# Kernel tuning notes

Hardware: AMD Instinct MI355X
Metric: run time of the kernel (lower is better)

Reference implementation:

```python
import jax, jax.numpy as jnp
import numpy as np

N = 500_000
N_GROUPS = 50_000
D_IN = 64
D_OUT = 64
IN_MLP = D_IN * 3  # x, x - min, x - max (use_num=False)
NEG_SLOPE = 0.2


def setup_inputs() -> dict:
    key = jax.random.key(0)
    k_x, k_c, k_w1, k_w2 = jax.random.split(key, 4)
    x = jax.random.normal(k_x, (N, D_IN), dtype=jnp.float32)
    # CSR pointer: 0 = p0 <= p1 <= ... <= p_{n_groups} = N
    inner = jnp.sort(jax.random.randint(k_c, (N_GROUPS - 1,), 0, N))
    csr_idx = jnp.concatenate([jnp.zeros((1,), jnp.int64 if jax.config.jax_enable_x64 else jnp.int32),
                               inner.astype(jnp.int32),
                               jnp.full((1,), N, jnp.int32)]).astype(jnp.int32)
    # MLP([in_mlp, d_out, d_out], bias=False): two bias-free Linear layers,
    # each followed by LeakyReLU(0.2) (BatchNorm omitted / identity).
    w1 = jax.random.normal(k_w1, (IN_MLP, D_OUT), dtype=jnp.float32) / np.sqrt(IN_MLP)
    w2 = jax.random.normal(k_w2, (D_OUT, D_OUT), dtype=jnp.float32) / np.sqrt(D_OUT)
    return {"x": x, "csr_idx": csr_idx, "w1": w1, "w2": w2}


def _forward(x, csr_idx, w1, w2):
    n = x.shape[0]
    # element -> segment id (jit-safe equivalent of repeat_interleave on lengths)
    seg = jnp.searchsorted(csr_idx, jnp.arange(n, dtype=csr_idx.dtype), side='right') - 1  # [N]
    # segment min/max + gather-back
    seg_min = jax.ops.segment_min(x, seg, num_segments=N_GROUPS)  # [G, D]
    seg_max = jax.ops.segment_max(x, seg, num_segments=N_GROUPS)  # [G, D]
    x_map_min = x - seg_min[seg]
    x_map_max = x - seg_max[seg]
    h = jnp.concatenate([x, x_map_min, x_map_max], axis=1)  # [N, 3*D_IN]
    h = jax.nn.leaky_relu(h @ w1, NEG_SLOPE)
    h = jax.nn.leaky_relu(h @ w2, NEG_SLOPE)
    return h


def reference(x, csr_idx, w1, w2):
    return _forward(x, csr_idx, w1, w2)
```

## Files before the change

### kernel.cpp

```cpp
#include <hip/hip_runtime.h>
#include <math.h>

#define NROWS 500000
#define NGRP  50000
#define NEG   0.2f
#define GPB   16

typedef __attribute__((ext_vector_type(8))) short bf16x8;
typedef __attribute__((ext_vector_type(4))) float f32x4;
typedef unsigned int uint32;

__device__ __forceinline__ float leaky(float h) { return fmaxf(h, NEG * h); }
__device__ __forceinline__ unsigned short f2bf(float v) {
    uint32 u = __float_as_uint(v);
    u += 0x7FFFu + ((u >> 16) & 1u);
    return (unsigned short)(u >> 16);
}
__device__ __forceinline__ float bf2f(unsigned short h) {
    return __uint_as_float((uint32)h << 16);
}
__device__ __forceinline__ uint32 pkbf(float a, float b) {
    uint32 r;
    asm("v_cvt_pk_bf16_f32 %0, %1, %2" : "=v"(r) : "v"(a), "v"(b));
    return r;
}

__global__ void k0_frag(const float* __restrict__ w1, const float* __restrict__ w2,
                        unsigned short* __restrict__ wsf, unsigned short* __restrict__ w2f,
                        unsigned short* __restrict__ wbh, unsigned short* __restrict__ wbl) {
    int r = blockIdx.x * 256 + threadIdx.x;
    if (r >= 8192) return;
    int j = r & 7, q = (r >> 3) & 3, n = (r >> 5) & 63;
    int k = (r >> 11) * 32 + q * 8 + j;
    if (r < 4096) {
        float ws = w1[k * 64 + n] + w1[4096 + k * 64 + n] + w1[8192 + k * 64 + n];
        wsf[r] = f2bf(ws);
        w2f[r] = f2bf(w2[k * 64 + n]);
    }
    float v = w1[(64 + k) * 64 + n];
    unsigned short h = f2bf(v);
    wbh[r] = h;
    wbl[r] = f2bf(v - bf2f(h));
}

__global__ __launch_bounds__(256, 6)
void grpstat(const float* __restrict__ x, const int* __restrict__ csr,
             const unsigned short* __restrict__ wbh,
             const unsigned short* __restrict__ wbl,
             float* __restrict__ biasG, int* __restrict__ seg) {
    __shared__ float mnF[GPB * 132];
    __shared__ int csrl[GPB + 1];

    const int tid = threadIdx.x, w = tid >> 6, lane = tid & 63;
    const int q = lane >> 4, nl = lane & 15;
    const int n = w * 16 + nl;

    const int g0 = blockIdx.x * GPB;
    if (tid <= GPB) csrl[tid] = csr[g0 + tid];
    __syncthreads();
    const int p0 = csrl[0], p1 = csrl[GPB];

    for (int r = p0 + tid; r < p1; r += 256) {
        int lo = 0, hi = GPB;
#pragma unroll
        for (int it = 0; it < 5; ++it) {
            int mid = (lo + hi) >> 1;
            bool cb = csrl[mid] <= r;
            lo = cb ? mid : lo;
            hi = cb ? hi : mid;
        }
        seg[r] = g0 + lo;
    }

    {
        const int sub = q;
        const float4* xr = (const float4*)x;

        auto redgrp = [&](int gl, int q0, int cnt,
                          float4 r0, float4 r1, float4 r2, float4 r3) {
            if (cnt <= 0) return;
            float4 mn, mx;
            mn.x = fminf(fminf(r0.x, r1.x), fminf(r2.x, r3.x));
            mn.y = fminf(fminf(r0.y, r1.y), fminf(r2.y, r3.y));
            mn.z = fminf(fminf(r0.z, r1.z), fminf(r2.z, r3.z));
            mn.w = fminf(fminf(r0.w, r1.w), fminf(r2.w, r3.w));
            mx.x = fmaxf(fmaxf(r0.x, r1.x), fmaxf(r2.x, r3.x));
            mx.y = fmaxf(fmaxf(r0.y, r1.y), fmaxf(r2.y, r3.y));
            mx.z = fmaxf(fmaxf(r0.z, r1.z), fmaxf(r2.z, r3.z));
            mx.w = fmaxf(fmaxf(r0.w, r1.w), fmaxf(r2.w, r3.w));
            for (int i = 16; i < cnt; i += 16) {
                int ra = q0 + min(i + sub,      cnt - 1);
                int rb = q0 + min(i + sub + 4,  cnt - 1);
                int rc = q0 + min(i + sub + 8,  cnt - 1);
                int rd = q0 + min(i + sub + 12, cnt - 1);
                float4 a = xr[ra * 16 + nl], b = xr[rb * 16 + nl];
                float4 c = xr[rc * 16 + nl], d = xr[rd * 16 + nl];
                mn.x = fminf(mn.x, fminf(fminf(a.x, b.x), fminf(c.x, d.x)));
                mn.y = fminf(mn.y, fminf(fminf(a.y, b.y), fminf(c.y, d.y)));
                mn.z = fminf(mn.z, fminf(fminf(a.z, b.z), fminf(c.z, d.z)));
                mn.w = fminf(mn.w, fminf(fminf(a.w, b.w), fminf(c.w, d.w)));
                mx.x = fmaxf(mx.x, fmaxf(fmaxf(a.x, b.x), fmaxf(c.x, d.x)));
                mx.y = fmaxf(mx.y, fmaxf(fmaxf(a.y, b.y), fmaxf(c.y, d.y)));
                mx.z = fmaxf(mx.z, fmaxf(fmaxf(a.z, b.z), fmaxf(c.z, d.z)));
                mx.w = fmaxf(mx.w, fmaxf(fmaxf(a.w, b.w), fmaxf(c.w, d.w)));
            }
#pragma unroll
            for (int mk = 16; mk <= 32; mk <<= 1) {
                mn.x = fminf(mn.x, __shfl_xor(mn.x, mk));
                mn.y = fminf(mn.y, __shfl_xor(mn.y, mk));
                mn.z = fminf(mn.z, __shfl_xor(mn.z, mk));
                mn.w = fminf(mn.w, __shfl_xor(mn.w, mk));
                mx.x = fmaxf(mx.x, __shfl_xor(mx.x, mk));
                mx.y = fmaxf(mx.y, __shfl_xor(mx.y, mk));
                mx.z = fmaxf(mx.z, __shfl_xor(mx.z, mk));
                mx.w = fmaxf(mx.w, __shfl_xor(mx.w, mk));
            }
            if (sub == 0) {
                *(float4*)&mnF[gl * 132 + nl * 4]      = mn;
                *(float4*)&mnF[gl * 132 + 64 + nl * 4] = mx;
            }
        };

#pragma unroll
        for (int pr = 0; pr < 2; ++pr) {
            const int gA = w + pr * 8, gB = gA + 4;
            int qA = csrl[gA], cA = csrl[gA + 1] - qA;
            int qB = csrl[gB], cB = csrl[gB + 1] - qB;
            const int bA = (cA > 0) ? qA : 0, iA = max(cA - 1, 0);
            const int bB = (cB > 0) ? qB : 0, iB = max(cB - 1, 0);
            float4 a0 = xr[(bA + min(sub,      iA)) * 16 + nl];
            float4 a1 = xr[(bA + min(sub + 4,  iA)) * 16 + nl];
            float4 a2 = xr[(bA + min(sub + 8,  iA)) * 16 + nl];
            float4 a3 = xr[(bA + min(sub + 12, iA)) * 16 + nl];
            float4 b0 = xr[(bB + min(sub,      iB)) * 16 + nl];
            float4 b1 = xr[(bB + min(sub + 4,  iB)) * 16 + nl];
            float4 b2 = xr[(bB + min(sub + 8,  iB)) * 16 + nl];
            float4 b3 = xr[(bB + min(sub + 12, iB)) * 16 + nl];
            redgrp(gA, qA, cA, a0, a1, a2, a3);
            redgrp(gB, qB, cB, b0, b1, b2, b3);
        }
    }
    __syncthreads();

    {
        const bf16x8* bhv = (const bf16x8*)wbh;
        const bf16x8* blv = (const bf16x8*)wbl;
        f32x4 acc = { 0.f, 0.f, 0.f, 0.f };
#pragma unroll
        for (int ks = 0; ks < 4; ++ks) {
            bf16x8 Bh = bhv[(ks * 64 + n) * 4 + q];
            bf16x8 Bl = blv[(ks * 64 + n) * 4 + q];
            const float* ap = &mnF[nl * 132 + ks * 32 + q * 8];
            f32x4 v0 = *(const f32x4*)ap;
            f32x4 v1 = *(const f32x4*)(ap + 4);
            union U { bf16x8 v; uint32 u[4]; } ah, al;
            ah.u[0] = pkbf(v0[0], v0[1]);
            ah.u[1] = pkbf(v0[2], v0[3]);
            ah.u[2] = pkbf(v1[0], v1[1]);
            ah.u[3] = pkbf(v1[2], v1[3]);
            float r0 = v0[0] - __uint_as_float(ah.u[0] << 16);
            float r1 = v0[1] - __uint_as_float(ah.u[0] & 0xffff0000u);
            float r2 = v0[2] - __uint_as_float(ah.u[1] << 16);
            float r3 = v0[3] - __uint_as_float(ah.u[1] & 0xffff0000u);
            float r4 = v1[0] - __uint_as_float(ah.u[2] << 16);
            float r5 = v1[1] - __uint_as_float(ah.u[2] & 0xffff0000u);
            float r6 = v1[2] - __uint_as_float(ah.u[3] << 16);
            float r7 = v1[3] - __uint_as_float(ah.u[3] & 0xffff0000u);
            al.u[0] = pkbf(r0, r1);
            al.u[1] = pkbf(r2, r3);
            al.u[2] = pkbf(r4, r5);
            al.u[3] = pkbf(r6, r7);
            acc = __builtin_amdgcn_mfma_f32_16x16x32_bf16(ah.v, Bh, acc, 0, 0, 0);
            acc = __builtin_amdgcn_mfma_f32_16x16x32_bf16(al.v, Bh, acc, 0, 0, 0);
            acc = __builtin_amdgcn_mfma_f32_16x16x32_bf16(ah.v, Bl, acc, 0, 0, 0);
        }
#pragma unroll
        for (int r = 0; r < 4; ++r)
            biasG[(size_t)(g0 + q * 4 + r) * 64 + n] = -acc[r];
    }
}

__global__ __launch_bounds__(256, 6)
void mlp(const float* __restrict__ x, const int* __restrict__ seg,
         const float* __restrict__ biasG,
         const unsigned short* __restrict__ wsf,
         const unsigned short* __restrict__ w2f,
         float* __restrict__ out) {
    __shared__ __align__(16) short xb[64 * 72];
    __shared__ __align__(16) short y1s[64 * 72];
    __shared__ __align__(16) int rowgrpL[64];

    const int tid = threadIdx.x, w = tid >> 6, lane = tid & 63;
    const int q = lane >> 4, nl = lane & 15;
    const int n = w * 16 + nl;

    const int r0 = blockIdx.x * 64;
    const int rows = min(64, NROWS - r0);
    const int availf = rows * 64;

    const float4* x4 = (const float4*)(x + (size_t)r0 * 64);
#pragma unroll
    for (int i = 0; i < 4; ++i) {
        int f = (i * 256 + tid) * 4;
        if (f < availf) {
            float4 v = x4[f >> 2];
            int r = f >> 6, c = f & 63;
            uint2 p;
            p.x = pkbf(v.x, v.y);
            p.y = pkbf(v.z, v.w);
            *(uint2*)(&xb[r * 72 + c]) = p;
        }
    }
    if (tid < 64) rowgrpL[tid] = seg[min(r0 + tid, NROWS - 1)];

    const bf16x8* wsv = (const bf16x8*)wsf;
    const bf16x8* w2v = (const bf16x8*)w2f;
    bf16x8 B0 = wsv[n * 4 + q];
    bf16x8 B1 = wsv[(64 + n) * 4 + q];
    bf16x8 C0 = w2v[n * 4 + q];
    bf16x8 C1 = w2v[(64 + n) * 4 + q];
    __syncthreads();

    f32x4 h[4];
#pragma unroll
    for (int mt = 0; mt < 4; ++mt) {
        int rbase = mt * 16 + q * 4;
        int4 grp = *(const int4*)(&rowgrpL[rbase]);
        f32x4 acc;
        acc.x = biasG[(size_t)grp.x * 64 + n];
        acc.y = biasG[(size_t)grp.y * 64 + n];
        acc.z = biasG[(size_t)grp.z * 64 + n];
        acc.w = biasG[(size_t)grp.w * 64 + n];
        bf16x8 a0 = *(const bf16x8*)(&xb[(mt * 16 + nl) * 72 + q * 8]);
        bf16x8 a1 = *(const bf16x8*)(&xb[(mt * 16 + nl) * 72 + 32 + q * 8]);
        acc = __builtin_amdgcn_mfma_f32_16x16x32_bf16(a0, B0, acc, 0, 0, 0);
        acc = __builtin_amdgcn_mfma_f32_16x16x32_bf16(a1, B1, acc, 0, 0, 0);
        h[mt] = acc;
    }
#pragma unroll
    for (int mt = 0; mt < 4; ++mt) {
        int rbase = mt * 16 + q * 4;
        uint32 p01 = pkbf(leaky(h[mt][0]), leaky(h[mt][1]));
        uint32 p23 = pkbf(leaky(h[mt][2]), leaky(h[mt][3]));
        y1s[(rbase + 0) * 72 + n] = (short)(p01 & 0xffffu);
        y1s[(rbase + 1) * 72 + n] = (short)(p01 >> 16);
        y1s[(rbase + 2) * 72 + n] = (short)(p23 & 0xffffu);
        y1s[(rbase + 3) * 72 + n] = (short)(p23 >> 16);
    }
    __syncthreads();

#pragma unroll
    for (int mt = 0; mt < 4; ++mt) {
        f32x4 acc = {0.f, 0.f, 0.f, 0.f};
        bf16x8 a0 = *(const bf16x8*)(&y1s[(mt * 16 + nl) * 72 + q * 8]);
        bf16x8 a1 = *(const bf16x8*)(&y1s[(mt * 16 + nl) * 72 + 32 + q * 8]);
        acc = __builtin_amdgcn_mfma_f32_16x16x32_bf16(a0, C0, acc, 0, 0, 0);
        acc = __builtin_amdgcn_mfma_f32_16x16x32_bf16(a1, C1, acc, 0, 0, 0);
        int rbase = mt * 16 + q * 4;
#pragma unroll
        for (int r = 0; r < 4; ++r) {
            int rl = rbase + r;
            if (rl < rows)
                out[(size_t)(r0 + rl) * 64 + n] = leaky(acc[r]);
        }
    }
}

extern "C" void kernel_launch(void* const* d_in, const int* in_sizes, int n_in,
                              void* d_out, int out_size, void* d_ws, size_t ws_size,
                              hipStream_t stream) {
    const float* x   = (const float*)d_in[0];
    const int*   csr = (const int*)d_in[1];
    const float* w1  = (const float*)d_in[2];
    const float* w2  = (const float*)d_in[3];
    float* out = (float*)d_out;

    unsigned short* wsf = (unsigned short*)d_ws;
    unsigned short* w2f = wsf + 4096;
    unsigned short* wbh = wsf + 8192;
    unsigned short* wbl = wsf + 16384;
    float* biasG = (float*)((char*)d_ws + 49152);
    int*   seg   = (int*)((char*)d_ws + 49152 + 12800000);

    k0_frag<<<32, 256, 0, stream>>>(w1, w2, wsf, w2f, wbh, wbl);
    grpstat<<<NGRP / GPB, 256, 0, stream>>>(x, csr, wbh, wbl, biasG, seg);
    mlp<<<(NROWS + 63) / 64, 256, 0, stream>>>(x, seg, biasG, wsf, w2f, out);
}
```

Baseline: 260.3 us.

## Fuse group-stat and MLP into one persistent cooperative kernel with prefetch

```diff
diff --git a/kernel.cpp b/kernel.cpp
--- a/kernel.cpp
+++ b/kernel.cpp
@@ -1,10 +1,13 @@
 #include <hip/hip_runtime.h>
+#include <hip/hip_cooperative_groups.h>
 #include <math.h>
 
 #define NROWS 500000
 #define NGRP  50000
 #define NEG   0.2f
 #define GPB   16
+#define NCHG  3125
+#define NCHR  7813
 
 typedef __attribute__((ext_vector_type(8))) short bf16x8;
 typedef __attribute__((ext_vector_type(4))) float f32x4;
@@ -43,22 +46,19 @@
     wbl[r] = f2bf(v - bf2f(h));
 }
 
-__global__ __launch_bounds__(256, 6)
-void grpstat(const float* __restrict__ x, const int* __restrict__ csr,
-             const unsigned short* __restrict__ wbh,
-             const unsigned short* __restrict__ wbl,
-             float* __restrict__ biasG, int* __restrict__ seg) {
-    __shared__ float mnF[GPB * 132];
-    __shared__ int csrl[GPB + 1];
-
-    const int tid = threadIdx.x, w = tid >> 6, lane = tid & 63;
-    const int q = lane >> 4, nl = lane & 15;
-    const int n = w * 16 + nl;
-
-    const int g0 = blockIdx.x * GPB;
+
+__device__ __forceinline__ void phase1_chunk(
+        int gc, const float* __restrict__ x, const int* __restrict__ csr,
+        const unsigned short* __restrict__ wbh,
+        const unsigned short* __restrict__ wbl,
+        float* __restrict__ biasG, int* __restrict__ seg,
+        float* mnF, int* csrl,
+        int tid, int w, int q, int nl, int n) {
+    const int g0 = gc * GPB;
     if (tid <= GPB) csrl[tid] = csr[g0 + tid];
     __syncthreads();
     const int p0 = csrl[0], p1 = csrl[GPB];
+    const float4* xr = (const float4*)x;
 
     for (int r = p0 + tid; r < p1; r += 256) {
         int lo = 0, hi = GPB;
@@ -74,8 +74,6 @@
 
     {
         const int sub = q;
-        const float4* xr = (const float4*)x;
-
         auto redgrp = [&](int gl, int q0, int cnt,
                           float4 r0, float4 r1, float4 r2, float4 r3) {
             if (cnt <= 0) return;
@@ -120,7 +118,6 @@
                 *(float4*)&mnF[gl * 132 + 64 + nl * 4] = mx;
             }
         };
-
 #pragma unroll
         for (int pr = 0; pr < 2; ++pr) {
             const int gA = w + pr * 8, gB = gA + 4;
@@ -180,30 +177,21 @@
     }
 }
 
-__global__ __launch_bounds__(256, 6)
-void mlp(const float* __restrict__ x, const int* __restrict__ seg,
-         const float* __restrict__ biasG,
-         const unsigned short* __restrict__ wsf,
-         const unsigned short* __restrict__ w2f,
-         float* __restrict__ out) {
-    __shared__ __align__(16) short xb[64 * 72];
-    __shared__ __align__(16) short y1s[64 * 72];
-    __shared__ __align__(16) int rowgrpL[64];
-
-    const int tid = threadIdx.x, w = tid >> 6, lane = tid & 63;
-    const int q = lane >> 4, nl = lane & 15;
-    const int n = w * 16 + nl;
-
-    const int r0 = blockIdx.x * 64;
+__device__ __forceinline__ void phase2_chunk(
+        int rc, int rn, float4 stg[4], const float* __restrict__ x,
+        const int* __restrict__ seg, const float* __restrict__ biasG,
+        bf16x8 B0, bf16x8 B1, bf16x8 C0, bf16x8 C1,
+        float* __restrict__ out, short* xb, short* y1s, int* rowgrpL,
+        int tid, int q, int nl, int n) {
+    const int r0 = rc * 64;
     const int rows = min(64, NROWS - r0);
     const int availf = rows * 64;
 
-    const float4* x4 = (const float4*)(x + (size_t)r0 * 64);
 #pragma unroll
     for (int i = 0; i < 4; ++i) {
         int f = (i * 256 + tid) * 4;
         if (f < availf) {
-            float4 v = x4[f >> 2];
+            float4 v = stg[i];
             int r = f >> 6, c = f & 63;
             uint2 p;
             p.x = pkbf(v.x, v.y);
@@ -212,16 +200,18 @@
         }
     }
     if (tid < 64) rowgrpL[tid] = seg[min(r0 + tid, NROWS - 1)];
-
-    const bf16x8* wsv = (const bf16x8*)wsf;
-    const bf16x8* w2v = (const bf16x8*)w2f;
-    bf16x8 B0 = wsv[n * 4 + q];
-    bf16x8 B1 = wsv[(64 + n) * 4 + q];
-    bf16x8 C0 = w2v[n * 4 + q];
-    bf16x8 C1 = w2v[(64 + n) * 4 + q];
     __syncthreads();
 
-    f32x4 h[4];
+    if (rn >= 0) {
+        const int availn = min(64, NROWS - rn * 64) * 64;
+        const float4* x4 = (const float4*)(x + (size_t)rn * 64 * 64);
+#pragma unroll
+        for (int i = 0; i < 4; ++i) {
+            int f = (i * 256 + tid) * 4;
+            if (f < availn) stg[i] = x4[f >> 2];
+        }
+    }
+
 #pragma unroll
     for (int mt = 0; mt < 4; ++mt) {
         int rbase = mt * 16 + q * 4;
@@ -235,13 +225,8 @@
         bf16x8 a1 = *(const bf16x8*)(&xb[(mt * 16 + nl) * 72 + 32 + q * 8]);
         acc = __builtin_amdgcn_mfma_f32_16x16x32_bf16(a0, B0, acc, 0, 0, 0);
         acc = __builtin_amdgcn_mfma_f32_16x16x32_bf16(a1, B1, acc, 0, 0, 0);
-        h[mt] = acc;
-    }
-#pragma unroll
-    for (int mt = 0; mt < 4; ++mt) {
-        int rbase = mt * 16 + q * 4;
-        uint32 p01 = pkbf(leaky(h[mt][0]), leaky(h[mt][1]));
-        uint32 p23 = pkbf(leaky(h[mt][2]), leaky(h[mt][3]));
+        uint32 p01 = pkbf(leaky(acc[0]), leaky(acc[1]));
+        uint32 p23 = pkbf(leaky(acc[2]), leaky(acc[3]));
         y1s[(rbase + 0) * 72 + n] = (short)(p01 & 0xffffu);
         y1s[(rbase + 1) * 72 + n] = (short)(p01 >> 16);
         y1s[(rbase + 2) * 72 + n] = (short)(p23 & 0xffffu);
@@ -264,6 +249,110 @@
                 out[(size_t)(r0 + rl) * 64 + n] = leaky(acc[r]);
         }
     }
+}
+
+__global__ __launch_bounds__(256, 6)
+void both(const float* __restrict__ x, const int* __restrict__ csr,
+          const unsigned short* __restrict__ wbh,
+          const unsigned short* __restrict__ wbl,
+          const unsigned short* __restrict__ wsf,
+          const unsigned short* __restrict__ w2f,
+          float* __restrict__ biasG, int* __restrict__ seg,
+          float* __restrict__ out) {
+    __shared__ __align__(16) char smem[18944];
+    float* mnF  = (float*)smem;
+    int*   csrl = (int*)(smem + 8448);
+    short* xb   = (short*)smem;
+    short* y1s  = (short*)(smem + 9216);
+    int*   rowgrpL = (int*)(smem + 18432);
+
+    const int tid = threadIdx.x, w = tid >> 6, lane = tid & 63;
+    const int q = lane >> 4, nl = lane & 15;
+    const int n = w * 16 + nl;
+    const int bid = blockIdx.x, gsz = gridDim.x;
+
+    for (int gc = bid; gc < NCHG; gc += gsz) {
+        phase1_chunk(gc, x, csr, wbh, wbl, biasG, seg, mnF, csrl,
+                     tid, w, q, nl, n);
+        __syncthreads();
+    }
+
+    int rc = bid;
+    float4 stg[4];
+    if (rc < NCHR) {
+        const int availf = min(64, NROWS - rc * 64) * 64;
+        const float4* x4 = (const float4*)(x + (size_t)rc * 64 * 64);
+#pragma unroll
+        for (int i = 0; i < 4; ++i) {
+            int f = (i * 256 + tid) * 4;
+            if (f < availf) stg[i] = x4[f >> 2];
+        }
+    }
+
+    __threadfence();
+    cooperative_groups::this_grid().sync();
+
+    const bf16x8* wsv = (const bf16x8*)wsf;
+    const bf16x8* w2v = (const bf16x8*)w2f;
+    bf16x8 B0 = wsv[n * 4 + q];
+    bf16x8 B1 = wsv[(64 + n) * 4 + q];
+    bf16x8 C0 = w2v[n * 4 + q];
+    bf16x8 C1 = w2v[(64 + n) * 4 + q];
+
+    while (rc < NCHR) {
+        int rn = rc + gsz;
+        phase2_chunk(rc, rn < NCHR ? rn : -1, stg, x, seg, biasG,
+                     B0, B1, C0, C1, out, xb, y1s, rowgrpL, tid, q, nl, n);
+        rc = rn;
+    }
+}
+
+__global__ __launch_bounds__(256, 6)
+void grpstat(const float* __restrict__ x, const int* __restrict__ csr,
+             const unsigned short* __restrict__ wbh,
+             const unsigned short* __restrict__ wbl,
+             float* __restrict__ biasG, int* __restrict__ seg) {
+    __shared__ __align__(16) float mnF[GPB * 132];
+    __shared__ int csrl[GPB + 1];
+    const int tid = threadIdx.x, w = tid >> 6, lane = tid & 63;
+    const int q = lane >> 4, nl = lane & 15;
+    const int n = w * 16 + nl;
+    phase1_chunk(blockIdx.x, x, csr, wbh, wbl, biasG, seg, mnF, csrl,
+                 tid, w, q, nl, n);
+}
+
+__global__ __launch_bounds__(256, 6)
+void mlp(const float* __restrict__ x, const int* __restrict__ seg,
+         const float* __restrict__ biasG,
+         const unsigned short* __restrict__ wsf,
+         const unsigned short* __restrict__ w2f,
+         float* __restrict__ out) {
+    __shared__ __align__(16) short xb[64 * 72];
+    __shared__ __align__(16) short y1s[64 * 72];
+    __shared__ __align__(16) int rowgrpL[64];
+    const int tid = threadIdx.x, w = tid >> 6, lane = tid & 63;
+    const int q = lane >> 4, nl = lane & 15;
+    const int n = w * 16 + nl;
+    const int rc = blockIdx.x;
+
+    float4 stg[4];
+    {
+        const int availf = min(64, NROWS - rc * 64) * 64;
+        const float4* x4 = (const float4*)(x + (size_t)rc * 64 * 64);
+#pragma unroll
+        for (int i = 0; i < 4; ++i) {
+            int f = (i * 256 + tid) * 4;
+            if (f < availf) stg[i] = x4[f >> 2];
+        }
+    }
+    const bf16x8* wsv = (const bf16x8*)wsf;
+    const bf16x8* w2v = (const bf16x8*)w2f;
+    bf16x8 B0 = wsv[n * 4 + q];
+    bf16x8 B1 = wsv[(64 + n) * 4 + q];
+    bf16x8 C0 = w2v[n * 4 + q];
+    bf16x8 C1 = w2v[(64 + n) * 4 + q];
+    phase2_chunk(rc, -1, stg, x, seg, biasG, B0, B1, C0, C1, out,
+                 xb, y1s, rowgrpL, tid, q, nl, n);
 }
 
 extern "C" void kernel_launch(void* const* d_in, const int* in_sizes, int n_in,
@@ -283,6 +372,35 @@
     int*   seg   = (int*)((char*)d_ws + 49152 + 12800000);
 
     k0_frag<<<32, 256, 0, stream>>>(w1, w2, wsf, w2f, wbh, wbl);
-    grpstat<<<NGRP / GPB, 256, 0, stream>>>(x, csr, wbh, wbl, biasG, seg);
-    mlp<<<(NROWS + 63) / 64, 256, 0, stream>>>(x, seg, biasG, wsf, w2f, out);
-}
+
+    static int coopGrid = -2;
+    if (coopGrid == -2) {
+        int nb = 0, ncu = 0, dev = 0;
+        if (hipGetDevice(&dev) == hipSuccess &&
+            hipDeviceGetAttribute(&ncu, hipDeviceAttributeMultiprocessorCount,
+                                  dev) == hipSuccess &&
+            hipOccupancyMaxActiveBlocksPerMultiprocessor(
+                &nb, (const void*)both, 256, 0) == hipSuccess &&
+            nb > 0 && ncu > 0) {
+            long g = (long)nb * ncu;
+            coopGrid = (int)(g < 1536 ? g : 1536);
+        } else {
+            coopGrid = -1;
+        }
+    }
+
+    bool launched = false;
+    if (coopGrid > 0) {
+        void* args[] = { (void*)&x, (void*)&csr, (void*)&wbh, (void*)&wbl,
+                         (void*)&wsf, (void*)&w2f, (void*)&biasG, (void*)&seg,
+                         (void*)&out };
+        launched = hipLaunchCooperativeKernel((const void*)both, dim3(coopGrid),
+                                              dim3(256), args, 0, stream)
+                   == hipSuccess;
+        if (!launched) coopGrid = -1;
+    }
+    if (!launched) {
+        grpstat<<<NCHG, 256, 0, stream>>>(x, csr, wbh, wbl, biasG, seg);
+        mlp<<<NCHR, 256, 0, stream>>>(x, seg, biasG, wsf, w2f, out);
+    }
+}
```

Result: slower. 450.0 us (+72.9%).

## Make MLP kernel persistent with register prefetch of next x tile

Applied to the files above, without the earlier changes.

```diff
diff --git a/kernel.cpp b/kernel.cpp
--- a/kernel.cpp
+++ b/kernel.cpp
@@ -5,6 +5,9 @@
 #define NGRP  50000
 #define NEG   0.2f
 #define GPB   16
+#define NCHG  3125
+#define NCHR  7813
+#define GRID2 1954
 
 typedef __attribute__((ext_vector_type(8))) short bf16x8;
 typedef __attribute__((ext_vector_type(4))) float f32x4;
@@ -43,22 +46,18 @@
     wbl[r] = f2bf(v - bf2f(h));
 }
 
-__global__ __launch_bounds__(256, 6)
-void grpstat(const float* __restrict__ x, const int* __restrict__ csr,
-             const unsigned short* __restrict__ wbh,
-             const unsigned short* __restrict__ wbl,
-             float* __restrict__ biasG, int* __restrict__ seg) {
-    __shared__ float mnF[GPB * 132];
-    __shared__ int csrl[GPB + 1];
-
-    const int tid = threadIdx.x, w = tid >> 6, lane = tid & 63;
-    const int q = lane >> 4, nl = lane & 15;
-    const int n = w * 16 + nl;
-
-    const int g0 = blockIdx.x * GPB;
+__device__ __forceinline__ void phase1_chunk(
+        int gc, const float* __restrict__ x, const int* __restrict__ csr,
+        const unsigned short* __restrict__ wbh,
+        const unsigned short* __restrict__ wbl,
+        float* __restrict__ biasG, int* __restrict__ seg,
+        float* mnF, int* csrl,
+        int tid, int w, int q, int nl, int n) {
+    const int g0 = gc * GPB;
     if (tid <= GPB) csrl[tid] = csr[g0 + tid];
     __syncthreads();
     const int p0 = csrl[0], p1 = csrl[GPB];
+    const float4* xr = (const float4*)x;
 
     for (int r = p0 + tid; r < p1; r += 256) {
         int lo = 0, hi = GPB;
@@ -74,8 +73,6 @@
 
     {
         const int sub = q;
-        const float4* xr = (const float4*)x;
-
         auto redgrp = [&](int gl, int q0, int cnt,
                           float4 r0, float4 r1, float4 r2, float4 r3) {
             if (cnt <= 0) return;
@@ -120,7 +117,6 @@
                 *(float4*)&mnF[gl * 132 + 64 + nl * 4] = mx;
             }
         };
-
 #pragma unroll
         for (int pr = 0; pr < 2; ++pr) {
             const int gA = w + pr * 8, gB = gA + 4;
@@ -181,6 +177,20 @@
 }
 
 __global__ __launch_bounds__(256, 6)
+void grpstat(const float* __restrict__ x, const int* __restrict__ csr,
+             const unsigned short* __restrict__ wbh,
+             const unsigned short* __restrict__ wbl,
+             float* __restrict__ biasG, int* __restrict__ seg) {
+    __shared__ __align__(16) float mnF[GPB * 132];
+    __shared__ int csrl[GPB + 1];
+    const int tid = threadIdx.x, w = tid >> 6, lane = tid & 63;
+    const int q = lane >> 4, nl = lane & 15;
+    const int n = w * 16 + nl;
+    phase1_chunk(blockIdx.x, x, csr, wbh, wbl, biasG, seg, mnF, csrl,
+                 tid, w, q, nl, n);
+}
+
+__global__ __launch_bounds__(256, 4)
 void mlp(const float* __restrict__ x, const int* __restrict__ seg,
          const float* __restrict__ biasG,
          const unsigned short* __restrict__ wsf,
@@ -188,30 +198,11 @@
          float* __restrict__ out) {
     __shared__ __align__(16) short xb[64 * 72];
     __shared__ __align__(16) short y1s[64 * 72];
-    __shared__ __align__(16) int rowgrpL[64];
 
     const int tid = threadIdx.x, w = tid >> 6, lane = tid & 63;
     const int q = lane >> 4, nl = lane & 15;
     const int n = w * 16 + nl;
-
-    const int r0 = blockIdx.x * 64;
-    const int rows = min(64, NROWS - r0);
-    const int availf = rows * 64;
-
-    const float4* x4 = (const float4*)(x + (size_t)r0 * 64);
-#pragma unroll
-    for (int i = 0; i < 4; ++i) {
-        int f = (i * 256 + tid) * 4;
-        if (f < availf) {
-            float4 v = x4[f >> 2];
-            int r = f >> 6, c = f & 63;
-            uint2 p;
-            p.x = pkbf(v.x, v.y);
-            p.y = pkbf(v.z, v.w);
-            *(uint2*)(&xb[r * 72 + c]) = p;
-        }
-    }
-    if (tid < 64) rowgrpL[tid] = seg[min(r0 + tid, NROWS - 1)];
+    const int stride = gridDim.x;
 
     const bf16x8* wsv = (const bf16x8*)wsf;
     const bf16x8* w2v = (const bf16x8*)w2f;
@@ -219,50 +210,108 @@
     bf16x8 B1 = wsv[(64 + n) * 4 + q];
     bf16x8 C0 = w2v[n * 4 + q];
     bf16x8 C1 = w2v[(64 + n) * 4 + q];
-    __syncthreads();
-
-    f32x4 h[4];
-#pragma unroll
-    for (int mt = 0; mt < 4; ++mt) {
-        int rbase = mt * 16 + q * 4;
-        int4 grp = *(const int4*)(&rowgrpL[rbase]);
-        f32x4 acc;
-        acc.x = biasG[(size_t)grp.x * 64 + n];
-        acc.y = biasG[(size_t)grp.y * 64 + n];
-        acc.z = biasG[(size_t)grp.z * 64 + n];
-        acc.w = biasG[(size_t)grp.w * 64 + n];
-        bf16x8 a0 = *(const bf16x8*)(&xb[(mt * 16 + nl) * 72 + q * 8]);
-        bf16x8 a1 = *(const bf16x8*)(&xb[(mt * 16 + nl) * 72 + 32 + q * 8]);
-        acc = __builtin_amdgcn_mfma_f32_16x16x32_bf16(a0, B0, acc, 0, 0, 0);
-        acc = __builtin_amdgcn_mfma_f32_16x16x32_bf16(a1, B1, acc, 0, 0, 0);
-        h[mt] = acc;
-    }
-#pragma unroll
-    for (int mt = 0; mt < 4; ++mt) {
-        int rbase = mt * 16 + q * 4;
-        uint32 p01 = pkbf(leaky(h[mt][0]), leaky(h[mt][1]));
-        uint32 p23 = pkbf(leaky(h[mt][2]), leaky(h[mt][3]));
-        y1s[(rbase + 0) * 72 + n] = (short)(p01 & 0xffffu);
-        y1s[(rbase + 1) * 72 + n] = (short)(p01 >> 16);
-        y1s[(rbase + 2) * 72 + n] = (short)(p23 & 0xffffu);
-        y1s[(rbase + 3) * 72 + n] = (short)(p23 >> 16);
-    }
-    __syncthreads();
-
-#pragma unroll
-    for (int mt = 0; mt < 4; ++mt) {
-        f32x4 acc = {0.f, 0.f, 0.f, 0.f};
-        bf16x8 a0 = *(const bf16x8*)(&y1s[(mt * 16 + nl) * 72 + q * 8]);
-        bf16x8 a1 = *(const bf16x8*)(&y1s[(mt * 16 + nl) * 72 + 32 + q * 8]);
-        acc = __builtin_amdgcn_mfma_f32_16x16x32_bf16(a0, C0, acc, 0, 0, 0);
-        acc = __builtin_amdgcn_mfma_f32_16x16x32_bf16(a1, C1, acc, 0, 0, 0);
-        int rbase = mt * 16 + q * 4;
-#pragma unroll
-        for (int r = 0; r < 4; ++r) {
-            int rl = rbase + r;
-            if (rl < rows)
-                out[(size_t)(r0 + rl) * 64 + n] = leaky(acc[r]);
-        }
+
+    int rc = blockIdx.x;
+    float4 stg[4];
+    {
+        const int availf = min(64, NROWS - rc * 64) * 64;
+        const float4* x4 = (const float4*)(x + (size_t)rc * 64 * 64);
+#pragma unroll
+        for (int i = 0; i < 4; ++i) {
+            int f = (i * 256 + tid) * 4;
+            if (f < availf) stg[i] = x4[f >> 2];
+        }
+    }
+
+    while (rc < NCHR) {
+        const int r0 = rc * 64;
+        const int rows = min(64, NROWS - r0);
+        const int availf = rows * 64;
+
+        int sg[16];
+#pragma unroll
+        for (int mt = 0; mt < 4; ++mt)
+#pragma unroll
+            for (int rr = 0; rr < 4; ++rr) {
+                int r = r0 + mt * 16 + q * 4 + rr;
+                sg[mt * 4 + rr] = seg[min(r, NROWS - 1)];
+            }
+
+#pragma unroll
+        for (int i = 0; i < 4; ++i) {
+            int f = (i * 256 + tid) * 4;
+            if (f < availf) {
+                float4 v = stg[i];
+                int r = f >> 6, c = f & 63;
+                uint2 p;
+                p.x = pkbf(v.x, v.y);
+                p.y = pkbf(v.z, v.w);
+                *(uint2*)(&xb[r * 72 + c]) = p;
+            }
+        }
+
+        float bias[16];
+#pragma unroll
+        for (int k = 0; k < 16; ++k)
+            bias[k] = biasG[(size_t)sg[k] * 64 + n];
+
+        __syncthreads();
+
+        const int rn = rc + stride;
+        if (rn < NCHR) {
+            const int availn = min(64, NROWS - rn * 64) * 64;
+            const float4* x4 = (const float4*)(x + (size_t)rn * 64 * 64);
+#pragma unroll
+            for (int i = 0; i < 4; ++i) {
+                int f = (i * 256 + tid) * 4;
+                if (f < availn) stg[i] = x4[f >> 2];
+            }
+        }
+
+#pragma unroll
+        for (int mt = 0; mt < 4; ++mt) {
+            int rbase = mt * 16 + q * 4;
+            f32x4 acc;
+            acc.x = bias[mt * 4 + 0];
+            acc.y = bias[mt * 4 + 1];
+            acc.z = bias[mt * 4 + 2];
+            acc.w = bias[mt * 4 + 3];
+            bf16x8 a0 = *(const bf16x8*)(&xb[(mt * 16 + nl) * 72 + q * 8]);
+            bf16x8 a1 = *(const bf16x8*)(&xb[(mt * 16 + nl) * 72 + 32 + q * 8]);
+            acc = __builtin_amdgcn_mfma_f32_16x16x32_bf16(a0, B0, acc, 0, 0, 0);
+            acc = __builtin_amdgcn_mfma_f32_16x16x32_bf16(a1, B1, acc, 0, 0, 0);
+            uint32 p01 = pkbf(leaky(acc[0]), leaky(acc[1]));
+            uint32 p23 = pkbf(leaky(acc[2]), leaky(acc[3]));
+            y1s[(rbase + 0) * 72 + n] = (short)(p01 & 0xffffu);
+            y1s[(rbase + 1) * 72 + n] = (short)(p01 >> 16);
+            y1s[(rbase + 2) * 72 + n] = (short)(p23 & 0xffffu);
+            y1s[(rbase + 3) * 72 + n] = (short)(p23 >> 16);
+        }
+        __syncthreads();
+
+        const bool full = (rows == 64);
+#pragma unroll
+        for (int mt = 0; mt < 4; ++mt) {
+            f32x4 acc = {0.f, 0.f, 0.f, 0.f};
+            bf16x8 a0 = *(const bf16x8*)(&y1s[(mt * 16 + nl) * 72 + q * 8]);
+            bf16x8 a1 = *(const bf16x8*)(&y1s[(mt * 16 + nl) * 72 + 32 + q * 8]);
+            acc = __builtin_amdgcn_mfma_f32_16x16x32_bf16(a0, C0, acc, 0, 0, 0);
+            acc = __builtin_amdgcn_mfma_f32_16x16x32_bf16(a1, C1, acc, 0, 0, 0);
+            int rbase = mt * 16 + q * 4;
+            if (full) {
+#pragma unroll
+                for (int rr = 0; rr < 4; ++rr)
+                    out[(size_t)(r0 + rbase + rr) * 64 + n] = leaky(acc[rr]);
+            } else {
+#pragma unroll
+                for (int rr = 0; rr < 4; ++rr) {
+                    int rl = rbase + rr;
+                    if (rl < rows)
+                        out[(size_t)(r0 + rl) * 64 + n] = leaky(acc[rr]);
+                }
+            }
+        }
+        rc = rn;
     }
 }
 
@@ -283,6 +332,6 @@
     int*   seg   = (int*)((char*)d_ws + 49152 + 12800000);
 
     k0_frag<<<32, 256, 0, stream>>>(w1, w2, wsf, w2f, wbh, wbl);
-    grpstat<<<NGRP / GPB, 256, 0, stream>>>(x, csr, wbh, wbl, biasG, seg);
-    mlp<<<(NROWS + 63) / 64, 256, 0, stream>>>(x, seg, biasG, wsf, w2f, out);
-}
+    grpstat<<<NCHG, 256, 0, stream>>>(x, csr, wbh, wbl, biasG, seg);
+    mlp<<<GRID2, 256, 0, stream>>>(x, seg, biasG, wsf, w2f, out);
+}
```

Result: slower. 268.1 us (+3.0%).

## Split group min/max into row-chunk scan plus per-group combine pass

Applied to the files above, without the earlier changes.

```diff
diff --git a/kernel.cpp b/kernel.cpp
--- a/kernel.cpp
+++ b/kernel.cpp
@@ -5,6 +5,8 @@
 #define NGRP  50000
 #define NEG   0.2f
 #define GPB   16
+#define NCHG  3125
+#define NCHR  7813
 
 typedef __attribute__((ext_vector_type(8))) short bf16x8;
 typedef __attribute__((ext_vector_type(4))) float f32x4;
@@ -23,6 +25,12 @@
     uint32 r;
     asm("v_cvt_pk_bf16_f32 %0, %1, %2" : "=v"(r) : "v"(a), "v"(b));
     return r;
+}
+__device__ __forceinline__ float4 min4(float4 a, float4 b) {
+    return float4{fminf(a.x,b.x), fminf(a.y,b.y), fminf(a.z,b.z), fminf(a.w,b.w)};
+}
+__device__ __forceinline__ float4 max4(float4 a, float4 b) {
+    return float4{fmaxf(a.x,b.x), fmaxf(a.y,b.y), fmaxf(a.z,b.z), fmaxf(a.w,b.w)};
 }
 
 __global__ void k0_frag(const float* __restrict__ w1, const float* __restrict__ w2,
@@ -43,102 +51,128 @@
     wbl[r] = f2bf(v - bf2f(h));
 }
 
+__global__ void segk(const int* __restrict__ csr, int* __restrict__ seg) {
+    int g = blockIdx.x * 256 + threadIdx.x;
+    if (g >= NGRP) return;
+    int p0 = csr[g], p1 = csr[g + 1];
+    for (int r = p0; r < p1; ++r) seg[r] = g;
+}
+
 __global__ __launch_bounds__(256, 6)
-void grpstat(const float* __restrict__ x, const int* __restrict__ csr,
+void s1_minmax(const float* __restrict__ x, const int* __restrict__ seg,
+               float* __restrict__ mnG, float* __restrict__ mxG,
+               float* __restrict__ hMn, float* __restrict__ hMx,
+               float* __restrict__ tMn, float* __restrict__ tMx) {
+    const int w = threadIdx.x >> 6, lane = threadIdx.x & 63;
+    const int wid = blockIdx.x * 4 + w;
+    if (wid >= NCHR) return;
+    const int w0 = wid << 6;
+    const int rows = min(64, NROWS - w0);
+    const float* __restrict__ xc = x + (size_t)w0 * 64 + lane;
+    const int segl = seg[min(w0 + lane, NROWS - 1)];
+
+    float vmn = INFINITY, vmx = -INFINITY;
+    int gcur = __shfl(segl, 0);
+    int runStart = 0;
+
+    auto flushRun = [&](bool atEnd) {
+        size_t ow = (size_t)wid * 64 + lane;
+        if (runStart == 0)      { hMn[ow] = vmn; hMx[ow] = vmx; }
+        else if (atEnd)         { tMn[ow] = vmn; tMx[ow] = vmx; }
+        else { size_t og = (size_t)gcur * 64 + lane; mnG[og] = vmn; mxG[og] = vmx; }
+    };
+
+    float v[8], nv[8];
+#define LD(buf, b)                                                          \
+    _Pragma("unroll")                                                       \
+    for (int j = 0; j < 8; ++j) buf[j] = xc[(size_t)((b) + j) * 64];
+#define PROC(buf, b)                                                        \
+    _Pragma("unroll")                                                       \
+    for (int j = 0; j < 8; ++j) {                                           \
+        int g = __shfl(segl, (b) + j);                                      \
+        if (g != gcur) {                                                    \
+            flushRun(false);                                                \
+            gcur = g; runStart = (b) + j; vmn = buf[j]; vmx = buf[j];       \
+        } else { vmn = fminf(vmn, buf[j]); vmx = fmaxf(vmx, buf[j]); }      \
+    }
+
+    LD(v, 0);
+    if (rows == 64) {
+#pragma unroll
+        for (int base = 0; base < 64; base += 16) {
+            if (base + 8 < 64)  { LD(nv, base + 8); }
+            PROC(v, base);
+            if (base + 16 < 64) { LD(v, base + 16); }
+            if (base + 8 < 64)  { PROC(nv, base + 8); }
+        }
+    } else {
+#pragma unroll
+        for (int base = 0; base < 32; base += 16) {
+            if (base + 8 < 32)  { LD(nv, base + 8); }
+            PROC(v, base);
+            if (base + 16 < 32) { LD(v, base + 16); }
+            if (base + 8 < 32)  { PROC(nv, base + 8); }
+        }
+    }
+#undef LD
+#undef PROC
+    flushRun(true);
+}
+
+__global__ __launch_bounds__(256, 6)
+void s2_bias(const int* __restrict__ csr,
+             const float* __restrict__ mnG, const float* __restrict__ mxG,
+             const float* __restrict__ hMn, const float* __restrict__ hMx,
+             const float* __restrict__ tMn, const float* __restrict__ tMx,
              const unsigned short* __restrict__ wbh,
              const unsigned short* __restrict__ wbl,
-             float* __restrict__ biasG, int* __restrict__ seg) {
+             float* __restrict__ biasG) {
     __shared__ float mnF[GPB * 132];
     __shared__ int csrl[GPB + 1];
 
     const int tid = threadIdx.x, w = tid >> 6, lane = tid & 63;
     const int q = lane >> 4, nl = lane & 15;
     const int n = w * 16 + nl;
-
     const int g0 = blockIdx.x * GPB;
+
     if (tid <= GPB) csrl[tid] = csr[g0 + tid];
     __syncthreads();
-    const int p0 = csrl[0], p1 = csrl[GPB];
-
-    for (int r = p0 + tid; r < p1; r += 256) {
-        int lo = 0, hi = GPB;
-#pragma unroll
-        for (int it = 0; it < 5; ++it) {
-            int mid = (lo + hi) >> 1;
-            bool cb = csrl[mid] <= r;
-            lo = cb ? mid : lo;
-            hi = cb ? hi : mid;
-        }
-        seg[r] = g0 + lo;
-    }
 
     {
-        const int sub = q;
-        const float4* xr = (const float4*)x;
-
-        auto redgrp = [&](int gl, int q0, int cnt,
-                          float4 r0, float4 r1, float4 r2, float4 r3) {
-            if (cnt <= 0) return;
-            float4 mn, mx;
-            mn.x = fminf(fminf(r0.x, r1.x), fminf(r2.x, r3.x));
-            mn.y = fminf(fminf(r0.y, r1.y), fminf(r2.y, r3.y));
-            mn.z = fminf(fminf(r0.z, r1.z), fminf(r2.z, r3.z));
-            mn.w = fminf(fminf(r0.w, r1.w), fminf(r2.w, r3.w));
-            mx.x = fmaxf(fmaxf(r0.x, r1.x), fmaxf(r2.x, r3.x));
-            mx.y = fmaxf(fmaxf(r0.y, r1.y), fmaxf(r2.y, r3.y));
-            mx.z = fmaxf(fmaxf(r0.z, r1.z), fmaxf(r2.z, r3.z));
-            mx.w = fmaxf(fmaxf(r0.w, r1.w), fmaxf(r2.w, r3.w));
-            for (int i = 16; i < cnt; i += 16) {
-                int ra = q0 + min(i + sub,      cnt - 1);
-                int rb = q0 + min(i + sub + 4,  cnt - 1);
-                int rc = q0 + min(i + sub + 8,  cnt - 1);
-                int rd = q0 + min(i + sub + 12, cnt - 1);
-                float4 a = xr[ra * 16 + nl], b = xr[rb * 16 + nl];
-                float4 c = xr[rc * 16 + nl], d = xr[rd * 16 + nl];
-                mn.x = fminf(mn.x, fminf(fminf(a.x, b.x), fminf(c.x, d.x)));
-                mn.y = fminf(mn.y, fminf(fminf(a.y, b.y), fminf(c.y, d.y)));
-                mn.z = fminf(mn.z, fminf(fminf(a.z, b.z), fminf(c.z, d.z)));
-                mn.w = fminf(mn.w, fminf(fminf(a.w, b.w), fminf(c.w, d.w)));
-                mx.x = fmaxf(mx.x, fmaxf(fmaxf(a.x, b.x), fmaxf(c.x, d.x)));
-                mx.y = fmaxf(mx.y, fmaxf(fmaxf(a.y, b.y), fmaxf(c.y, d.y)));
-                mx.z = fmaxf(mx.z, fmaxf(fmaxf(a.z, b.z), fmaxf(c.z, d.z)));
-                mx.w = fmaxf(mx.w, fmaxf(fmaxf(a.w, b.w), fmaxf(c.w, d.w)));
+        const int gl = tid >> 4, cq = tid & 15;
+        const int gg = g0 + gl;
+        const int s = csrl[gl], e = csrl[gl + 1];
+        float4 mn = { INFINITY, INFINITY, INFINITY, INFINITY };
+        float4 mx = { -INFINITY, -INFINITY, -INFINITY, -INFINITY };
+        if (s < e) {
+            const int wis = s >> 6, wie = (e - 1) >> 6;
+            const int weS = min((wis << 6) + 64, NROWS);
+            if (wis == wie && s != (wis << 6) && e != weS) {
+                mn = ((const float4*)(mnG + (size_t)gg * 64))[cq];
+                mx = ((const float4*)(mxG + (size_t)gg * 64))[cq];
+            } else {
+                for (int wi = wis; wi <= wie; ++wi) {
+                    const int ws_ = wi << 6;
+                    const int we_ = min(ws_ + 64, NROWS);
+                    const int a = max(s, ws_), b = min(e, we_);
+                    const float4 *pm, *px;
+                    if (a == ws_) {
+                        pm = (const float4*)(hMn + (size_t)wi * 64) + cq;
+                        px = (const float4*)(hMx + (size_t)wi * 64) + cq;
+                    } else if (b == we_) {
+                        pm = (const float4*)(tMn + (size_t)wi * 64) + cq;
+                        px = (const float4*)(tMx + (size_t)wi * 64) + cq;
+                    } else {
+                        pm = (const float4*)(mnG + (size_t)gg * 64) + cq;
+                        px = (const float4*)(mxG + (size_t)gg * 64) + cq;
+                    }
+                    mn = min4(mn, *pm);
+                    mx = max4(mx, *px);
+                }
             }
-#pragma unroll
-            for (int mk = 16; mk <= 32; mk <<= 1) {
-                mn.x = fminf(mn.x, __shfl_xor(mn.x, mk));
-                mn.y = fminf(mn.y, __shfl_xor(mn.y, mk));
-                mn.z = fminf(mn.z, __shfl_xor(mn.z, mk));
-                mn.w = fminf(mn.w, __shfl_xor(mn.w, mk));
-                mx.x = fmaxf(mx.x, __shfl_xor(mx.x, mk));
-                mx.y = fmaxf(mx.y, __shfl_xor(mx.y, mk));
-                mx.z = fmaxf(mx.z, __shfl_xor(mx.z, mk));
-                mx.w = fmaxf(mx.w, __shfl_xor(mx.w, mk));
-            }
-            if (sub == 0) {
-                *(float4*)&mnF[gl * 132 + nl * 4]      = mn;
-                *(float4*)&mnF[gl * 132 + 64 + nl * 4] = mx;
-            }
-        };
-
-#pragma unroll
-        for (int pr = 0; pr < 2; ++pr) {
-            const int gA = w + pr * 8, gB = gA + 4;
-            int qA = csrl[gA], cA = csrl[gA + 1] - qA;
-            int qB = csrl[gB], cB = csrl[gB + 1] - qB;
-            const int bA = (cA > 0) ? qA : 0, iA = max(cA - 1, 0);
-            const int bB = (cB > 0) ? qB : 0, iB = max(cB - 1, 0);
-            float4 a0 = xr[(bA + min(sub,      iA)) * 16 + nl];
-            float4 a1 = xr[(bA + min(sub + 4,  iA)) * 16 + nl];
-            float4 a2 = xr[(bA + min(sub + 8,  iA)) * 16 + nl];
-            float4 a3 = xr[(bA + min(sub + 12, iA)) * 16 + nl];
-            float4 b0 = xr[(bB + min(sub,      iB)) * 16 + nl];
-            float4 b1 = xr[(bB + min(sub + 4,  iB)) * 16 + nl];
-            float4 b2 = xr[(bB + min(sub + 8,  iB)) * 16 + nl];
-            float4 b3 = xr[(bB + min(sub + 12, iB)) * 16 + nl];
-            redgrp(gA, qA, cA, a0, a1, a2, a3);
-            redgrp(gB, qB, cB, b0, b1, b2, b3);
-        }
+        }
+        *(float4*)&mnF[gl * 132 + cq * 4]      = mn;
+        *(float4*)&mnF[gl * 132 + 64 + cq * 4] = mx;
     }
     __syncthreads();
 
@@ -180,6 +214,134 @@
     }
 }
 
+__device__ __forceinline__ void phase1_chunk(
+        int gc, const float* __restrict__ x, const int* __restrict__ csr,
+        const unsigned short* __restrict__ wbh,
+        const unsigned short* __restrict__ wbl,
+        float* __restrict__ biasG, int* __restrict__ seg,
+        float* mnF, int* csrl,
+        int tid, int w, int q, int nl, int n) {
+    const int g0 = gc * GPB;
+    if (tid <= GPB) csrl[tid] = csr[g0 + tid];
+    __syncthreads();
+    const int p0 = csrl[0], p1 = csrl[GPB];
+    const float4* xr = (const float4*)x;
+    for (int r = p0 + tid; r < p1; r += 256) {
+        int lo = 0, hi = GPB;
+#pragma unroll
+        for (int it = 0; it < 5; ++it) {
+            int mid = (lo + hi) >> 1;
+            bool cb = csrl[mid] <= r;
+            lo = cb ? mid : lo;
+            hi = cb ? hi : mid;
+        }
+        seg[r] = g0 + lo;
+    }
+    {
+        const int sub = q;
+        auto redgrp = [&](int gl, int q0, int cnt,
+                          float4 r0, float4 r1, float4 r2, float4 r3) {
+            if (cnt <= 0) return;
+            float4 mn = min4(min4(r0, r1), min4(r2, r3));
+            float4 mx = max4(max4(r0, r1), max4(r2, r3));
+            for (int i = 16; i < cnt; i += 16) {
+                int ra = q0 + min(i + sub,      cnt - 1);
+                int rb = q0 + min(i + sub + 4,  cnt - 1);
+                int rc = q0 + min(i + sub + 8,  cnt - 1);
+                int rd = q0 + min(i + sub + 12, cnt - 1);
+                float4 a = xr[ra * 16 + nl], b = xr[rb * 16 + nl];
+                float4 c = xr[rc * 16 + nl], d = xr[rd * 16 + nl];
+                mn = min4(mn, min4(min4(a, b), min4(c, d)));
+                mx = max4(mx, max4(max4(a, b), max4(c, d)));
+            }
+#pragma unroll
+            for (int mk = 16; mk <= 32; mk <<= 1) {
+                mn.x = fminf(mn.x, __shfl_xor(mn.x, mk));
+                mn.y = fminf(mn.y, __shfl_xor(mn.y, mk));
+                mn.z = fminf(mn.z, __shfl_xor(mn.z, mk));
+                mn.w = fminf(mn.w, __shfl_xor(mn.w, mk));
+                mx.x = fmaxf(mx.x, __shfl_xor(mx.x, mk));
+                mx.y = fmaxf(mx.y, __shfl_xor(mx.y, mk));
+                mx.z = fmaxf(mx.z, __shfl_xor(mx.z, mk));
+                mx.w = fmaxf(mx.w, __shfl_xor(mx.w, mk));
+            }
+            if (sub == 0) {
+                *(float4*)&mnF[gl * 132 + nl * 4]      = mn;
+                *(float4*)&mnF[gl * 132 + 64 + nl * 4] = mx;
+            }
+        };
+#pragma unroll
+        for (int pr = 0; pr < 2; ++pr) {
+            const int gA = w + pr * 8, gB = gA + 4;
+            int qA = csrl[gA], cA = csrl[gA + 1] - qA;
+            int qB = csrl[gB], cB = csrl[gB + 1] - qB;
+            const int bA = (cA > 0) ? qA : 0, iA = max(cA - 1, 0);
+            const int bB = (cB > 0) ? qB : 0, iB = max(cB - 1, 0);
+            float4 a0 = xr[(bA + min(sub,      iA)) * 16 + nl];
+            float4 a1 = xr[(bA + min(sub + 4,  iA)) * 16 + nl];
+            float4 a2 = xr[(bA + min(sub + 8,  iA)) * 16 + nl];
+            float4 a3 = xr[(bA + min(sub + 12, iA)) * 16 + nl];
+            float4 b0 = xr[(bB + min(sub,      iB)) * 16 + nl];
+            float4 b1 = xr[(bB + min(sub + 4,  iB)) * 16 + nl];
+            float4 b2 = xr[(bB + min(sub + 8,  iB)) * 16 + nl];
+            float4 b3 = xr[(bB + min(sub + 12, iB)) * 16 + nl];
+            redgrp(gA, qA, cA, a0, a1, a2, a3);
+            redgrp(gB, qB, cB, b0, b1, b2, b3);
+        }
+    }
+    __syncthreads();
+    {
+        const bf16x8* bhv = (const bf16x8*)wbh;
+        const bf16x8* blv = (const bf16x8*)wbl;
+        f32x4 acc = { 0.f, 0.f, 0.f, 0.f };
+#pragma unroll
+        for (int ks = 0; ks < 4; ++ks) {
+            bf16x8 Bh = bhv[(ks * 64 + n) * 4 + q];
+            bf16x8 Bl = blv[(ks * 64 + n) * 4 + q];
+            const float* ap = &mnF[nl * 132 + ks * 32 + q * 8];
+            f32x4 v0 = *(const f32x4*)ap;
+            f32x4 v1 = *(const f32x4*)(ap + 4);
+            union U { bf16x8 v; uint32 u[4]; } ah, al;
+            ah.u[0] = pkbf(v0[0], v0[1]);
+            ah.u[1] = pkbf(v0[2], v0[3]);
+            ah.u[2] = pkbf(v1[0], v1[1]);
+            ah.u[3] = pkbf(v1[2], v1[3]);
+            float r0 = v0[0] - __uint_as_float(ah.u[0] << 16);
+            float r1 = v0[1] - __uint_as_float(ah.u[0] & 0xffff0000u);
+            float r2 = v0[2] - __uint_as_float(ah.u[1] << 16);
+            float r3 = v0[3] - __uint_as_float(ah.u[1] & 0xffff0000u);
+            float r4 = v1[0] - __uint_as_float(ah.u[2] << 16);
+            float r5 = v1[1] - __uint_as_float(ah.u[2] & 0xffff0000u);
+            float r6 = v1[2] - __uint_as_float(ah.u[3] << 16);
+            float r7 = v1[3] - __uint_as_float(ah.u[3] & 0xffff0000u);
+            al.u[0] = pkbf(r0, r1);
+            al.u[1] = pkbf(r2, r3);
+            al.u[2] = pkbf(r4, r5);
+            al.u[3] = pkbf(r6, r7);
+            acc = __builtin_amdgcn_mfma_f32_16x16x32_bf16(ah.v, Bh, acc, 0, 0, 0);
+            acc = __builtin_amdgcn_mfma_f32_16x16x32_bf16(al.v, Bh, acc, 0, 0, 0);
+            acc = __builtin_amdgcn_mfma_f32_16x16x32_bf16(ah.v, Bl, acc, 0, 0, 0);
+        }
+#pragma unroll
+        for (int r = 0; r < 4; ++r)
+            biasG[(size_t)(g0 + q * 4 + r) * 64 + n] = -acc[r];
+    }
+}
+
+__global__ __launch_bounds__(256, 6)
+void grpstat(const float* __restrict__ x, const int* __restrict__ csr,
+             const unsigned short* __restrict__ wbh,
+             const unsigned short* __restrict__ wbl,
+             float* __restrict__ biasG, int* __restrict__ seg) {
+    __shared__ __align__(16) float mnF[GPB * 132];
+    __shared__ int csrl[GPB + 1];
+    const int tid = threadIdx.x, w = tid >> 6, lane = tid & 63;
+    const int q = lane >> 4, nl = lane & 15;
+    const int n = w * 16 + nl;
+    phase1_chunk(blockIdx.x, x, csr, wbh, wbl, biasG, seg, mnF, csrl,
+                 tid, w, q, nl, n);
+}
+
 __global__ __launch_bounds__(256, 6)
 void mlp(const float* __restrict__ x, const int* __restrict__ seg,
          const float* __restrict__ biasG,
@@ -275,14 +437,31 @@
     const float* w2  = (const float*)d_in[3];
     float* out = (float*)d_out;
 
-    unsigned short* wsf = (unsigned short*)d_ws;
-    unsigned short* w2f = wsf + 4096;
-    unsigned short* wbh = wsf + 8192;
-    unsigned short* wbl = wsf + 16384;
-    float* biasG = (float*)((char*)d_ws + 49152);
-    int*   seg   = (int*)((char*)d_ws + 49152 + 12800000);
+    char* base = (char*)d_ws;
+    unsigned short* wsf = (unsigned short*)base;
+    unsigned short* w2f = (unsigned short*)(base + 8192);
+    unsigned short* wbh = (unsigned short*)(base + 16384);
+    unsigned short* wbl = (unsigned short*)(base + 32768);
+    float* biasG = (float*)(base + 49152);
+    int*   seg   = (int*)(base + 49152 + 12800000);
+    float* mnG = (float*)(base + 14849152);
+    float* mxG = (float*)(base + 27649152);
+    float* hMn = (float*)(base + 40449152);
+    float* hMx = (float*)(base + 42449280);
+    float* tMn = (float*)(base + 44449408);
+    float* tMx = (float*)(base + 46449536);
+    const size_t need = 48449664ull;
 
     k0_frag<<<32, 256, 0, stream>>>(w1, w2, wsf, w2f, wbh, wbl);
-    grpstat<<<NGRP / GPB, 256, 0, stream>>>(x, csr, wbh, wbl, biasG, seg);
-    mlp<<<(NROWS + 63) / 64, 256, 0, stream>>>(x, seg, biasG, wsf, w2f, out);
-}
+
+    if (ws_size >= need) {
+        segk<<<(NGRP + 255) / 256, 256, 0, stream>>>(csr, seg);
+        s1_minmax<<<(NCHR + 3) / 4, 256, 0, stream>>>(x, seg, mnG, mxG,
+                                                      hMn, hMx, tMn, tMx);
+        s2_bias<<<NCHG, 256, 0, stream>>>(csr, mnG, mxG, hMn, hMx, tMn, tMx,
+                                          wbh, wbl, biasG);
+    } else {
+        grpstat<<<NCHG, 256, 0, stream>>>(x, csr, wbh, wbl, biasG, seg);
+    }
+    mlp<<<NCHR, 256, 0, stream>>>(x, seg, biasG, wsf, w2f, out);
+}
```

Measured after the change: 287.8 us. 1.11x slower.
